# Optimization experiments

Hardware: AMD Instinct MI355X
Metric: run time of the kernel (lower is better)

Reference implementation:

```python
import jax, jax.numpy as jnp
import numpy as np

B, N, C, H = 4, 4096, 1024, 16
D = C // H


def setup_inputs() -> dict:
    key = jax.random.key(0)
    ks = jax.random.split(key, 15)
    s = 0.02
    f = lambda k, shp: jax.random.normal(k, shp, dtype=jnp.float32) * s
    return {
        "x": f(ks[0], (B, N, C)),
        "qkv_w": f(ks[1], (C, 3 * C)),
        "qkv_b": f(ks[2], (3 * C,)),
        "out_w": f(ks[3], (C, C)),
        "out_b": f(ks[4], (C,)),
        # NB: original code dynamically re-creates position_bias as (1, N, H, H)
        # because q/k/v are never transposed to (B,H,N,D); attention runs over heads.
        "pos_bias": f(ks[5], (1, N, H, H)),
        "conv_w": f(ks[6], (C, C)),
        "conv_b": f(ks[7], (C,)),
        "pw_w": f(ks[8], (C, C, 1)),   # Conv1d kernel_size=1: (out, in, k)
        "pw_b": f(ks[9], (C,)),
        "dw_w": f(ks[10], (C, 1, 3)),  # depthwise Conv1d groups=C: (out, in/groups=1, k)
        "dw_b": f(ks[11], (C,)),
        "tok_w": f(ks[12], (C, C)),
        "tok_b": f(ks[13], (C,)),
    }


def reference(x, qkv_w, qkv_b, out_w, out_b, pos_bias,
              conv_w, conv_b, pw_w, pw_b, dw_w, dw_b, tok_w, tok_b):
    b, n, c = x.shape
    h = pos_bias.shape[2]
    d = c // h
    scale = d ** (-0.5)

    # ---- attention branch (faithful to source: heads axis is attended over) ----
    qkv = (x @ qkv_w + qkv_b).reshape(b, n, h, 3 * d)
    q, k, v = jnp.split(qkv, 3, axis=-1)  # each (B, N, H, D)
    scores = jnp.einsum("bnhd,bngd->bnhg", q, k) * scale + pos_bias  # (B, N, H, H)
    attn_w = jax.nn.softmax(scores, axis=-1)
    attn = jnp.einsum("bnhg,bngd->bnhd", attn_w, v).reshape(b, n, c)
    attn = attn @ out_w + out_b

    # ---- convolutional branch ----
    xc = x @ conv_w + conv_b            # (B, N, C)
    xc = xc.transpose(0, 2, 1)          # (B, C, N)
    dn = ("NCH", "OIH", "NCH")
    xc = jax.lax.conv_general_dilated(xc, pw_w, (1,), [(0, 0)],
                                      dimension_numbers=dn) + pw_b[None, :, None]
    xc = jax.lax.conv_general_dilated(xc, dw_w, (1,), [(1, 1)],
                                      dimension_numbers=dn,
                                      feature_group_count=c) + dw_b[None, :, None]
    xc = xc.transpose(0, 2, 1) @ tok_w + tok_b  # (B, N, C)

    return attn + xc
```

## Files before the change

kernel.cpp:

```cpp
#include <hip/hip_runtime.h>
#include <hip/hip_bf16.h>


typedef __attribute__((ext_vector_type(8))) short sh8;
typedef __attribute__((ext_vector_type(4))) float f4;

__device__ __forceinline__ float bf2f(short s) {
  unsigned u = ((unsigned)(unsigned short)s) << 16;
  return __builtin_bit_cast(float, u);
}
__device__ __forceinline__ short f2bf(float f) {
  return __builtin_bit_cast(short, __float2bfloat16(f));
}
__device__ __forceinline__ void g2l16(const void* g, void* l) {
  __builtin_amdgcn_global_load_lds(
      (const __attribute__((address_space(1))) unsigned int*)g,
      (__attribute__((address_space(3))) unsigned int*)l, 16, 0, 0);
}

__global__ __launch_bounds__(256) void cvt_f32_bf16(
    const float* __restrict__ src, short* __restrict__ dst, int n8) {
  int i = blockIdx.x * 256 + threadIdx.x;
  if (i >= n8) return;
  float4 a = ((const float4*)src)[i * 2];
  float4 b = ((const float4*)src)[i * 2 + 1];
  sh8 o;
  o[0] = f2bf(a.x); o[1] = f2bf(a.y); o[2] = f2bf(a.z); o[3] = f2bf(a.w);
  o[4] = f2bf(b.x); o[5] = f2bf(b.y); o[6] = f2bf(b.z); o[7] = f2bf(b.w);
  ((sh8*)dst)[i] = o;
}

__global__ __launch_bounds__(256) void transpose_f32_bf16(
    const float* __restrict__ src, short* __restrict__ dst,
    int N, int ldd, int coff) {
  __shared__ float tile[32][33];
  int kb = blockIdx.y * 32, nb = blockIdx.x * 32;
  int tx = threadIdx.x, ty = threadIdx.y;
#pragma unroll
  for (int j = 0; j < 32; j += 8)
    tile[ty + j][tx] = src[(size_t)(kb + ty + j) * N + nb + tx];
  __syncthreads();
#pragma unroll
  for (int j = 0; j < 32; j += 8)
    dst[(size_t)(nb + ty + j) * ldd + coff + kb + tx] = f2bf(tile[tx][ty + j]);
}

__global__ __launch_bounds__(256) void prep_misc(
    const float* __restrict__ pw_w, const float* __restrict__ conv_b,
    const float* __restrict__ pw_b, const float* __restrict__ out_b,
    const float* __restrict__ tok_b, const float* __restrict__ dw_w,
    const float* __restrict__ dw_b,
    float* __restrict__ b2, float* __restrict__ bcat,
    float* __restrict__ dw0, float* __restrict__ dw1,
    float* __restrict__ dw2, float* __restrict__ dwb) {
  int o = blockIdx.x;
  float part = 0.f;
  for (int i = threadIdx.x; i < 1024; i += 256)
    part += pw_w[(size_t)o * 1024 + i] * conv_b[i];
#pragma unroll
  for (int off = 32; off >= 1; off >>= 1) part += __shfl_down(part, off);
  __shared__ float red[4];
  int wid = threadIdx.x >> 6, lane = threadIdx.x & 63;
  if (lane == 0) red[wid] = part;
  __syncthreads();
  if (threadIdx.x == 0) {
    float s = red[0] + red[1] + red[2] + red[3];
    b2[o] = s + pw_b[o];
    bcat[o] = out_b[o] + tok_b[o];
    dw0[o] = dw_w[o * 3 + 0];
    dw1[o] = dw_w[o * 3 + 1];
    dw2[o] = dw_w[o * 3 + 2];
    dwb[o] = dw_b[o];
  }
}

template <int OUT_BF16>
__global__ __launch_bounds__(256, 2) void gemm128(
    const short* __restrict__ A, const short* __restrict__ Bt,
    void* __restrict__ Cp, const float* __restrict__ bias, int K, int ldc) {
  __shared__ short As[128 * 32];
  __shared__ short Bs[128 * 32];
  const int wid = threadIdx.x >> 6, lane = threadIdx.x & 63;
  const int bm = blockIdx.y, bn = blockIdx.x;
  const int wr = wid >> 1, wc = wid & 1;
  const size_t abase = (size_t)bm * 128 * K;
  const size_t bbase = (size_t)bn * 128 * K;
  const int r16 = lane & 15, ko = (lane >> 4) * 8;

  f4 acc[4][4] = {};

  for (int k0 = 0; k0 < K; k0 += 32) {
    __syncthreads();
#pragma unroll
    for (int c = 0; c < 2; ++c) {
      int ch = c * 256 + wid * 64 + lane;
      int row = ch >> 2, kc = (ch & 3) * 8;
      g2l16(A + abase + (size_t)row * K + k0 + kc, &As[ch * 8]);
      g2l16(Bt + bbase + (size_t)row * K + k0 + kc, &Bs[ch * 8]);
    }
    __syncthreads();
    sh8 af[4], bf[4];
#pragma unroll
    for (int i = 0; i < 4; ++i)
      af[i] = *(const sh8*)&As[(wr * 64 + i * 16 + r16) * 32 + ko];
#pragma unroll
    for (int j = 0; j < 4; ++j)
      bf[j] = *(const sh8*)&Bs[(wc * 64 + j * 16 + r16) * 32 + ko];
#pragma unroll
    for (int i = 0; i < 4; ++i)
#pragma unroll
      for (int j = 0; j < 4; ++j)
        acc[i][j] = __builtin_amdgcn_mfma_f32_16x16x32_bf16(af[i], bf[j],
                                                            acc[i][j], 0, 0, 0);
  }

  const int crow = wr * 64 + (lane >> 4) * 4;
  const int ccol = wc * 64 + r16;
#pragma unroll
  for (int i = 0; i < 4; ++i) {
#pragma unroll
    for (int j = 0; j < 4; ++j) {
      int col = bn * 128 + ccol + j * 16;
      float bv = bias ? bias[col] : 0.f;
#pragma unroll
      for (int r = 0; r < 4; ++r) {
        int row = bm * 128 + crow + i * 16 + r;
        float v = acc[i][j][r] + bv;
        if (OUT_BF16)
          ((short*)Cp)[(size_t)row * ldc + col] = f2bf(v);
        else
          ((float*)Cp)[(size_t)row * ldc + col] = v;
      }
    }
  }
}

template <int OUT_BF16>
__global__ __launch_bounds__(512, 2) void gemm256(
    const short* __restrict__ A, const short* __restrict__ Bt,
    void* __restrict__ Cp, const float* __restrict__ bias,
    int K, int ldc, int nbn) {
  __shared__ short lds[65536];
  const int tid = threadIdx.x;
  const int lane = tid & 63, wid = tid >> 6;
  const int wr = wid >> 2, wc = wid & 3;
  const int r16 = lane & 15;
  const int kidx = ((lane >> 4) ^ ((r16 >> 1) & 3)) << 3;

  const int cpx = gridDim.x >> 3;
  const int swz = (blockIdx.x & 7) * cpx + (blockIdx.x >> 3);
  const int bm = swz / nbn, bn = swz % nbn;

  const short* Ag = A + (size_t)bm * 256 * K;
  const short* Bg = Bt + (size_t)bn * 256 * K;

  int goff0, goff1, loff0, loff1;
  {
    int s0 = tid, row0 = s0 >> 2;
    int kc0 = (s0 & 3) ^ ((row0 >> 1) & 3);
    goff0 = row0 * K + kc0 * 8;
    loff0 = s0 * 8;
    int s1 = 512 + tid, row1 = s1 >> 2;
    int kc1 = (s1 & 3) ^ ((row1 >> 1) & 3);
    goff1 = row1 * K + kc1 * 8;
    loff1 = s1 * 8;
  }

  f4 acc[8][4] = {};
  const int NT = K >> 5;

#define STAGE(KT, B)                                        \
  do {                                                      \
    short* lb = &lds[(B) * 16384];                          \
    const short* ga = Ag + (KT) * 32;                       \
    const short* gb = Bg + (KT) * 32;                       \
    g2l16(ga + goff0, lb + loff0);                          \
    g2l16(gb + goff0, lb + 8192 + loff0);                   \
    g2l16(ga + goff1, lb + loff1);                          \
    g2l16(gb + goff1, lb + 8192 + loff1);                   \
  } while (0)

  STAGE(0, 0);
  STAGE(1, 1);

  for (int t = 0; t < NT; ++t) {
    asm volatile("s_waitcnt vmcnt(4)" ::: "memory");
    __builtin_amdgcn_sched_barrier(0);
    __builtin_amdgcn_s_barrier();
    const int kt2 = (t + 2 < NT) ? t + 2 : 0;
    STAGE(kt2, (t + 2) & 3);

    const short* Ab = &lds[(t & 3) * 16384];
    const short* Bb = Ab + 8192;
    sh8 af[8], bfr[4];
#pragma unroll
    for (int i = 0; i < 8; ++i)
      af[i] = *(const sh8*)&Ab[(wr * 128 + i * 16 + r16) * 32 + kidx];
#pragma unroll
    for (int j = 0; j < 4; ++j)
      bfr[j] = *(const sh8*)&Bb[(wc * 64 + j * 16 + r16) * 32 + kidx];
    __builtin_amdgcn_s_setprio(1);
#pragma unroll
    for (int i = 0; i < 8; ++i)
#pragma unroll
      for (int j = 0; j < 4; ++j)
        acc[i][j] = __builtin_amdgcn_mfma_f32_16x16x32_bf16(af[i], bfr[j],
                                                            acc[i][j], 0, 0, 0);
    __builtin_amdgcn_s_setprio(0);
  }
#undef STAGE

  const int crow0 = bm * 256 + wr * 128 + (lane >> 4) * 4;
  const int ccol0 = bn * 256 + wc * 64 + r16;
#pragma unroll
  for (int j = 0; j < 4; ++j) {
    int col = ccol0 + j * 16;
    float bv = bias ? bias[col] : 0.f;
#pragma unroll
    for (int i = 0; i < 8; ++i) {
      int rowb = crow0 + i * 16;
#pragma unroll
      for (int r = 0; r < 4; ++r) {
        float v = acc[i][j][r] + bv;
        if (OUT_BF16)
          ((short*)Cp)[(size_t)(rowb + r) * ldc + col] = f2bf(v);
        else
          ((float*)Cp)[(size_t)(rowb + r) * ldc + col] = v;
      }
    }
  }
}

__global__ __launch_bounds__(256) void attn_fused(
    const short* __restrict__ qkv, const float* __restrict__ pos_bias,
    short* __restrict__ xcat) {
  __shared__ short sq[4 * 3072];
  int t0 = blockIdx.x * 4;
  const sh8* gsrc = (const sh8*)(qkv + (size_t)t0 * 3072);
  sh8* ldst = (sh8*)sq;
#pragma unroll
  for (int c = 0; c < 6; ++c) ldst[threadIdx.x + c * 256] = gsrc[threadIdx.x + c * 256];
  __syncthreads();

  int wid = threadIdx.x >> 6, lane = threadIdx.x & 63;
  int t = t0 + wid, n = t & 4095;
  int h = lane >> 2, sub = lane & 3;
  const short* base = sq + wid * 3072 + h * 192;

  float qf[64];
#pragma unroll
  for (int c = 0; c < 8; ++c) {
    sh8 v8 = *(const sh8*)(base + c * 8);
#pragma unroll
    for (int j = 0; j < 8; ++j) qf[c * 8 + j] = bf2f(v8[j]);
  }

  const float* pb = pos_bias + (size_t)n * 256 + h * 16 + sub * 4;
  float p[4];
  float m = -1e30f;
#pragma unroll
  for (int g4 = 0; g4 < 4; ++g4) {
    int g = sub * 4 + g4;
    const short* kk = sq + wid * 3072 + g * 192 + 64;
    float acc = 0.f;
#pragma unroll
    for (int c = 0; c < 8; ++c) {
      sh8 k8 = *(const sh8*)(kk + c * 8);
#pragma unroll
      for (int j = 0; j < 8; ++j) acc += qf[c * 8 + j] * bf2f(k8[j]);
    }
    p[g4] = acc * 0.125f + pb[g4];
    m = fmaxf(m, p[g4]);
  }
  m = fmaxf(m, __shfl_xor(m, 1));
  m = fmaxf(m, __shfl_xor(m, 2));
  float sum = 0.f;
#pragma unroll
  for (int g4 = 0; g4 < 4; ++g4) {
    p[g4] = __expf(p[g4] - m);
    sum += p[g4];
  }
  sum += __shfl_xor(sum, 1);
  sum += __shfl_xor(sum, 2);
  float inv = 1.0f / sum;
#pragma unroll
  for (int g4 = 0; g4 < 4; ++g4) p[g4] *= inv;

  float pall[16];
#pragma unroll
  for (int g = 0; g < 16; ++g)
    pall[g] = __shfl(p[g & 3], (lane & 60) | (g >> 2));

  float o[16] = {};
#pragma unroll
  for (int g = 0; g < 16; ++g) {
    const short* vv = sq + wid * 3072 + g * 192 + 128 + sub * 16;
    sh8 va = *(const sh8*)vv;
    sh8 vb = *(const sh8*)(vv + 8);
#pragma unroll
    for (int j = 0; j < 8; ++j) {
      o[j] += pall[g] * bf2f(va[j]);
      o[8 + j] += pall[g] * bf2f(vb[j]);
    }
  }
  sh8 oa, ob;
#pragma unroll
  for (int j = 0; j < 8; ++j) {
    oa[j] = f2bf(o[j]);
    ob[j] = f2bf(o[8 + j]);
  }
  short* dst = xcat + (size_t)t * 2048 + h * 64 + sub * 16;
  *(sh8*)dst = oa;
  *(sh8*)(dst + 8) = ob;
}

__global__ __launch_bounds__(256) void dwconv(
    const short* __restrict__ xc2, const float* __restrict__ dw0,
    const float* __restrict__ dw1, const float* __restrict__ dw2,
    const float* __restrict__ dwb, short* __restrict__ xcat) {
  int idx = blockIdx.x * 256 + threadIdx.x;
  int t = idx >> 7, c = (idx & 127) * 8;
  int n = t & 4095;
  const short* row = xc2 + (size_t)t * 1024 + c;
  sh8 mid = *(const sh8*)row;
  sh8 lo = {}, hi = {};
  if (n > 0) lo = *(const sh8*)(row - 1024);
  if (n < 4095) hi = *(const sh8*)(row + 1024);
  sh8 out;
#pragma unroll
  for (int j = 0; j < 8; ++j) {
    float v = dw0[c + j] * bf2f(lo[j]) + dw1[c + j] * bf2f(mid[j]) +
              dw2[c + j] * bf2f(hi[j]) + dwb[c + j];
    out[j] = f2bf(v);
  }
  *(sh8*)(xcat + (size_t)t * 2048 + 1024 + c) = out;
}

extern "C" void kernel_launch(void* const* d_in, const int* in_sizes, int n_in,
                              void* d_out, int out_size, void* d_ws,
                              size_t ws_size, hipStream_t stream) {
  const float* x      = (const float*)d_in[0];
  const float* qkv_w  = (const float*)d_in[1];
  const float* qkv_b  = (const float*)d_in[2];
  const float* out_w  = (const float*)d_in[3];
  const float* out_b  = (const float*)d_in[4];
  const float* pos_b  = (const float*)d_in[5];
  const float* conv_w = (const float*)d_in[6];
  const float* conv_b = (const float*)d_in[7];
  const float* pw_w   = (const float*)d_in[8];
  const float* pw_b   = (const float*)d_in[9];
  const float* dw_w   = (const float*)d_in[10];
  const float* dw_b   = (const float*)d_in[11];
  const float* tok_w  = (const float*)d_in[12];
  const float* tok_b  = (const float*)d_in[13];

  const int M = 16384;
  char* ws = (char*)d_ws;
  size_t off = 0;
  auto alloc = [&](size_t bytes) -> void* {
    void* p = ws + off;
    off += (bytes + 255) & ~(size_t)255;
    return p;
  };
  short* xb    = (short*)alloc((size_t)M * 1024 * 2);
  short* qkvwt = (short*)alloc((size_t)3072 * 1024 * 2);
  short* wcatT = (short*)alloc((size_t)1024 * 2048 * 2);
  short* convb = (short*)alloc((size_t)1024 * 1024 * 2);
  short* pwb   = (short*)alloc((size_t)1024 * 1024 * 2);
  short* w2t   = (short*)alloc((size_t)1024 * 1024 * 2);
  short* qkvb  = (short*)alloc((size_t)M * 3072 * 2);
  short* xc2   = (short*)alloc((size_t)M * 1024 * 2);
  short* xcat  = (short*)alloc((size_t)M * 2048 * 2);
  float* b2    = (float*)alloc(1024 * 4);
  float* bcat  = (float*)alloc(1024 * 4);
  float* dw0   = (float*)alloc(1024 * 4);
  float* dw1   = (float*)alloc(1024 * 4);
  float* dw2   = (float*)alloc(1024 * 4);
  float* dwb   = (float*)alloc(1024 * 4);
  (void)ws_size; (void)in_sizes; (void)n_in; (void)out_size;

  cvt_f32_bf16<<<8192, 256, 0, stream>>>(x, xb, M * 1024 / 8);
  cvt_f32_bf16<<<512, 256, 0, stream>>>(conv_w, convb, 1024 * 1024 / 8);
  cvt_f32_bf16<<<512, 256, 0, stream>>>(pw_w, pwb, 1024 * 1024 / 8);
  transpose_f32_bf16<<<dim3(96, 32), dim3(32, 8), 0, stream>>>(qkv_w, qkvwt, 3072, 1024, 0);
  transpose_f32_bf16<<<dim3(32, 32), dim3(32, 8), 0, stream>>>(out_w, wcatT, 1024, 2048, 0);
  transpose_f32_bf16<<<dim3(32, 32), dim3(32, 8), 0, stream>>>(tok_w, wcatT, 1024, 2048, 1024);
  prep_misc<<<1024, 256, 0, stream>>>(pw_w, conv_b, pw_b, out_b, tok_b, dw_w,
                                      dw_b, b2, bcat, dw0, dw1, dw2, dwb);
  gemm128<1><<<dim3(8, 8), 256, 0, stream>>>(pwb, convb, w2t, nullptr, 1024, 1024);

  gemm256<1><<<768, 512, 0, stream>>>(xb, qkvwt, qkvb, qkv_b, 1024, 3072, 12);
  gemm256<1><<<256, 512, 0, stream>>>(xb, w2t, xc2, b2, 1024, 1024, 4);

  attn_fused<<<4096, 256, 0, stream>>>(qkvb, pos_b, xcat);
  dwconv<<<8192, 256, 0, stream>>>(xc2, dw0, dw1, dw2, dwb, xcat);

  gemm256<0><<<256, 512, 0, stream>>>(xcat, wcatT, d_out, bcat, 2048, 1024, 4);
}
```

Measured before the change: 359.4 us.

## Split GEMM K-step into two MFMA phases interleaved with global-to-LDS loads

Restructures the GEMM main loop into two halves. Each half loads four A fragments, issues half of the next stage's global-to-LDS copies, then runs its MFMAs between barriers, in a ping-pong style schedule. The aim is to overlap LDS reads and global loads with matrix math and to spread memory issue across the iteration. The epilogue loop is also reordered so stores walk rows with hoisted bias values. The change adds extra barriers per iteration, which may cost more than the overlap gains.

```diff
diff --git a/kernel.cpp b/kernel.cpp
--- a/kernel.cpp
+++ b/kernel.cpp
@@ -169,7 +169,7 @@
   f4 acc[8][4] = {};
   const int NT = K >> 5;
 
-#define STAGE(KT, B)                                        \
+#define STAGE_FULL(KT, B)                                   \
   do {                                                      \
     short* lb = &lds[(B) * 16384];                          \
     const short* ga = Ag + (KT) * 32;                       \
@@ -180,52 +180,85 @@
     g2l16(gb + goff1, lb + 8192 + loff1);                   \
   } while (0)
 
-  STAGE(0, 0);
-  STAGE(1, 1);
+  STAGE_FULL(0, 0);
+  STAGE_FULL(1, 1);
+  asm volatile("s_waitcnt vmcnt(4)" ::: "memory");
+  __builtin_amdgcn_sched_barrier(0);
+  __builtin_amdgcn_s_barrier();
 
   for (int t = 0; t < NT; ++t) {
-    asm volatile("s_waitcnt vmcnt(4)" ::: "memory");
-    __builtin_amdgcn_sched_barrier(0);
-    __builtin_amdgcn_s_barrier();
-    const int kt2 = (t + 2 < NT) ? t + 2 : 0;
-    STAGE(kt2, (t + 2) & 3);
-
     const short* Ab = &lds[(t & 3) * 16384];
     const short* Bb = Ab + 8192;
+    const int kt2 = (t + 2 < NT) ? t + 2 : 0;
+    short* lb2 = &lds[((t + 2) & 3) * 16384];
+    const short* ga2 = Ag + kt2 * 32;
+    const short* gb2 = Bg + kt2 * 32;
+
     sh8 af[8], bfr[4];
-#pragma unroll
-    for (int i = 0; i < 8; ++i)
+
+#pragma unroll
+    for (int i = 0; i < 4; ++i)
       af[i] = *(const sh8*)&Ab[(wr * 128 + i * 16 + r16) * 32 + kidx];
 #pragma unroll
     for (int j = 0; j < 4; ++j)
       bfr[j] = *(const sh8*)&Bb[(wc * 64 + j * 16 + r16) * 32 + kidx];
+    g2l16(ga2 + goff0, lb2 + loff0);
+    g2l16(gb2 + goff0, lb2 + 8192 + loff0);
+    __builtin_amdgcn_sched_barrier(0);
+    __builtin_amdgcn_s_barrier();
+    asm volatile("s_waitcnt lgkmcnt(0)" ::: "memory");
+    __builtin_amdgcn_sched_barrier(0);
     __builtin_amdgcn_s_setprio(1);
 #pragma unroll
-    for (int i = 0; i < 8; ++i)
+    for (int i = 0; i < 4; ++i)
 #pragma unroll
       for (int j = 0; j < 4; ++j)
         acc[i][j] = __builtin_amdgcn_mfma_f32_16x16x32_bf16(af[i], bfr[j],
                                                             acc[i][j], 0, 0, 0);
     __builtin_amdgcn_s_setprio(0);
-  }
-#undef STAGE
+    __builtin_amdgcn_sched_barrier(0);
+    __builtin_amdgcn_s_barrier();
+
+#pragma unroll
+    for (int i = 4; i < 8; ++i)
+      af[i] = *(const sh8*)&Ab[(wr * 128 + i * 16 + r16) * 32 + kidx];
+    g2l16(ga2 + goff1, lb2 + loff1);
+    g2l16(gb2 + goff1, lb2 + 8192 + loff1);
+    __builtin_amdgcn_sched_barrier(0);
+    __builtin_amdgcn_s_barrier();
+    asm volatile("s_waitcnt lgkmcnt(0)" ::: "memory");
+    __builtin_amdgcn_sched_barrier(0);
+    __builtin_amdgcn_s_setprio(1);
+#pragma unroll
+    for (int i = 4; i < 8; ++i)
+#pragma unroll
+      for (int j = 0; j < 4; ++j)
+        acc[i][j] = __builtin_amdgcn_mfma_f32_16x16x32_bf16(af[i], bfr[j],
+                                                            acc[i][j], 0, 0, 0);
+    __builtin_amdgcn_s_setprio(0);
+    __builtin_amdgcn_sched_barrier(0);
+    asm volatile("s_waitcnt vmcnt(4)" ::: "memory");
+    __builtin_amdgcn_s_barrier();
+  }
+#undef STAGE_FULL
 
   const int crow0 = bm * 256 + wr * 128 + (lane >> 4) * 4;
   const int ccol0 = bn * 256 + wc * 64 + r16;
-#pragma unroll
-  for (int j = 0; j < 4; ++j) {
-    int col = ccol0 + j * 16;
-    float bv = bias ? bias[col] : 0.f;
-#pragma unroll
-    for (int i = 0; i < 8; ++i) {
-      int rowb = crow0 + i * 16;
-#pragma unroll
-      for (int r = 0; r < 4; ++r) {
-        float v = acc[i][j][r] + bv;
+  float bv[4];
+#pragma unroll
+  for (int j = 0; j < 4; ++j) bv[j] = bias ? bias[ccol0 + j * 16] : 0.f;
+#pragma unroll
+  for (int i = 0; i < 8; ++i) {
+#pragma unroll
+    for (int r = 0; r < 4; ++r) {
+      size_t rowoff = (size_t)(crow0 + i * 16 + r) * ldc + ccol0;
+#pragma unroll
+      for (int j = 0; j < 4; ++j) {
+        float v = acc[i][j][r] + bv[j];
         if (OUT_BF16)
-          ((short*)Cp)[(size_t)(rowb + r) * ldc + col] = f2bf(v);
+          ((short*)Cp)[rowoff + j * 16] = f2bf(v);
         else
-          ((float*)Cp)[(size_t)(rowb + r) * ldc + col] = v;
+          ((float*)Cp)[rowoff + j * 16] = v;
       }
     }
   }
```

Result: faster. 343.2 us (-4.5%).
